# Performance work log

Hardware: AMD Instinct MI355X
Metric: run time of the kernel (lower is better)

## Reference

```python
import jax, jax.numpy as jnp
import numpy as np

EMBED_DIM = 1024
NUM_HEADS = 16
HEAD_DIM = EMBED_DIM // NUM_HEADS
SCALE = HEAD_DIM ** -0.5


def setup_inputs() -> dict:
    key = jax.random.key(0)
    ks = jax.random.split(key, 12)
    B, S, D = 2, 2048, EMBED_DIM
    w_std = D ** -0.5
    return {
        "query": jax.random.normal(ks[0], (B, S, D), jnp.float32),
        "key": jax.random.normal(ks[1], (B, S, D), jnp.float32),
        "value": jax.random.normal(ks[2], (B, S, D), jnp.float32),
        "mask": jnp.ones((B, S, S), jnp.int32),
        "Wq": jax.random.normal(ks[3], (D, D), jnp.float32) * w_std,
        "bq": jnp.zeros((D,), jnp.float32),
        "Wk": jax.random.normal(ks[4], (D, D), jnp.float32) * w_std,
        "bk": jnp.zeros((D,), jnp.float32),
        "Wv": jax.random.normal(ks[5], (D, D), jnp.float32) * w_std,
        "bv": jnp.zeros((D,), jnp.float32),
        "Wo": jax.random.normal(ks[6], (D, D), jnp.float32) * w_std,
        "bo": jnp.zeros((D,), jnp.float32),
    }


def reference(query, key, value, mask, Wq, bq, Wk, bk, Wv, bv, Wo, bo):
    B, Sq, D = query.shape
    H, Hd = NUM_HEADS, HEAD_DIM
    # projections (torch Linear: x @ W.T + b), then split heads -> [B, H, S, Hd]
    q = (query @ Wq.T + bq).reshape(B, Sq, H, Hd).transpose(0, 2, 1, 3)
    k = (key @ Wk.T + bk).reshape(B, -1, H, Hd).transpose(0, 2, 1, 3)
    v = (value @ Wv.T + bv).reshape(B, -1, H, Hd).transpose(0, 2, 1, 3)
    # scaled dot-product scores [B, H, Sq, Sk]
    scores = jnp.einsum("bhqd,bhkd->bhqk", q, k) * SCALE
    scores = jnp.where(mask[:, None, :, :] == 0, -1e9, scores)
    attn_weights = jax.nn.softmax(scores, axis=-1)
    # dropout rate = 0.0 -> identity in this configuration
    attn_output = jnp.einsum("bhqk,bhkd->bhqd", attn_weights, v)
    attn_output = attn_output.transpose(0, 2, 1, 3).reshape(B, Sq, D)
    output = attn_output @ Wo.T + bo
    return (output, attn_weights)
```

## Files before the change

kernel.cpp:

```cpp
#include <hip/hip_runtime.h>
#include <stdint.h>

#define B_ 2
#define S_ 2048
#define D_ 1024
#define H_ 16
#define HD_ 64
#define NT_ (S_ / 64)
#define SC2_ 0.18033688011112042f

typedef __bf16 bf16_t;
typedef bf16_t bf16x8 __attribute__((ext_vector_type(8)));
typedef float f32x4 __attribute__((ext_vector_type(4)));
typedef unsigned short u16x8 __attribute__((ext_vector_type(8)));
typedef unsigned short u16x4 __attribute__((ext_vector_type(4)));

static __device__ __forceinline__ unsigned short f2b(float f) {
  return __builtin_bit_cast(unsigned short, (bf16_t)f);
}

static __device__ __forceinline__ bf16x8 asb(u16x8 u) {
  return __builtin_bit_cast(bf16x8, u);
}

__global__ void cast3(const float* __restrict__ a, const float* __restrict__ b,
                      const float* __restrict__ c,
                      unsigned short* __restrict__ dst, int n) {
  const float* src = blockIdx.y == 0 ? a : (blockIdx.y == 1 ? b : c);
  unsigned short* d = dst + (size_t)blockIdx.y * n;
  int i = (blockIdx.x * blockDim.x + threadIdx.x) * 8;
  if (i >= n) return;
  float4 f0 = *(const float4*)(src + i);
  float4 f1 = *(const float4*)(src + i + 4);
  u16x8 o;
  o[0] = f2b(f0.x); o[1] = f2b(f0.y); o[2] = f2b(f0.z); o[3] = f2b(f0.w);
  o[4] = f2b(f1.x); o[5] = f2b(f1.y); o[6] = f2b(f1.z); o[7] = f2b(f1.w);
  *(u16x8*)(d + i) = o;
}

__global__ void cast4(const float* __restrict__ a, const float* __restrict__ b,
                      const float* __restrict__ c, const float* __restrict__ e,
                      unsigned short* __restrict__ dst, int n) {
  const float* src = blockIdx.y == 0 ? a
                   : (blockIdx.y == 1 ? b : (blockIdx.y == 2 ? c : e));
  unsigned short* d = dst + (size_t)blockIdx.y * n;
  int i = (blockIdx.x * blockDim.x + threadIdx.x) * 8;
  if (i >= n) return;
  float4 f0 = *(const float4*)(src + i);
  float4 f1 = *(const float4*)(src + i + 4);
  u16x8 o;
  o[0] = f2b(f0.x); o[1] = f2b(f0.y); o[2] = f2b(f0.z); o[3] = f2b(f0.w);
  o[4] = f2b(f1.x); o[5] = f2b(f1.y); o[6] = f2b(f1.z); o[7] = f2b(f1.w);
  *(u16x8*)(d + i) = o;
}

__global__ void pack_mask(const int* __restrict__ mask,
                          uint32_t* __restrict__ mbits) {
  int i = blockIdx.x * blockDim.x + threadIdx.x;
  unsigned long long bits = __ballot(mask[i] != 0);
  if ((threadIdx.x & 63) == 0)
    *(unsigned long long*)&mbits[i >> 5] = bits;
}

template<int OUTMODE>
__global__ __launch_bounds__(256)
void gemm_bt(const unsigned short* __restrict__ Ab,
             const unsigned short* __restrict__ Wb,
             const float* __restrict__ bq_,
             const float* __restrict__ bk_,
             const float* __restrict__ bv_,
             void* __restrict__ outv,
             int M, int N, int K) {
  const int z = blockIdx.z;
  const unsigned short* A = Ab + (size_t)z * M * K;
  const unsigned short* W = Wb + (size_t)z * N * K;
  const float* bias = z == 0 ? bq_ : (z == 1 ? bk_ : bv_);

  __shared__ __align__(16) unsigned short As[128 * 40];
  __shared__ __align__(16) unsigned short Bs[128 * 40];

  const int tid = threadIdx.x;
  const int lane = tid & 63;
  const int wave = tid >> 6;
  const int wm = wave >> 1, wn = wave & 1;
  const int row0 = blockIdx.x * 128;
  const int col0 = blockIdx.y * 128;

  const int srow = tid >> 2;
  const int scol = (tid & 3) * 8;
  const int lr = lane & 15;
  const int lg = lane >> 4;
  const int lk = lg * 8;

  f32x4 acc[4][4] = {};

  u16x8 a0 = *(const u16x8*)&A[(size_t)(row0 + srow) * K + scol];
  u16x8 a1 = *(const u16x8*)&A[(size_t)(row0 + srow + 64) * K + scol];
  u16x8 b0 = *(const u16x8*)&W[(size_t)(col0 + srow) * K + scol];
  u16x8 b1 = *(const u16x8*)&W[(size_t)(col0 + srow + 64) * K + scol];

  for (int k0 = 0; k0 < K; k0 += 32) {
    __syncthreads();
    *(u16x8*)&As[srow * 40 + scol] = a0;
    *(u16x8*)&As[(srow + 64) * 40 + scol] = a1;
    *(u16x8*)&Bs[srow * 40 + scol] = b0;
    *(u16x8*)&Bs[(srow + 64) * 40 + scol] = b1;
    if (k0 + 32 < K) {
      a0 = *(const u16x8*)&A[(size_t)(row0 + srow) * K + k0 + 32 + scol];
      a1 = *(const u16x8*)&A[(size_t)(row0 + srow + 64) * K + k0 + 32 + scol];
      b0 = *(const u16x8*)&W[(size_t)(col0 + srow) * K + k0 + 32 + scol];
      b1 = *(const u16x8*)&W[(size_t)(col0 + srow + 64) * K + k0 + 32 + scol];
    }
    __syncthreads();

    bf16x8 af[4], bfr[4];
#pragma unroll
    for (int i = 0; i < 4; ++i)
      af[i] = asb(*(const u16x8*)&As[(wm * 64 + i * 16 + lr) * 40 + lk]);
#pragma unroll
    for (int j = 0; j < 4; ++j)
      bfr[j] = asb(*(const u16x8*)&Bs[(wn * 64 + j * 16 + lr) * 40 + lk]);
#pragma unroll
    for (int i = 0; i < 4; ++i)
#pragma unroll
      for (int j = 0; j < 4; ++j)
        acc[i][j] = __builtin_amdgcn_mfma_f32_16x16x32_bf16(af[i], bfr[j], acc[i][j], 0, 0, 0);
  }

  const size_t zo = (size_t)z * M * N;
#pragma unroll
  for (int i = 0; i < 4; ++i) {
#pragma unroll
    for (int j = 0; j < 4; ++j) {
      const int row_ = row0 + wm * 64 + i * 16 + lg * 4;
      const int col = col0 + wn * 64 + j * 16 + lr;
      const float bcol = bias[col];
      if (OUTMODE == 1) {
        float* O = (float*)outv;
#pragma unroll
        for (int r = 0; r < 4; ++r)
          __builtin_nontemporal_store(acc[i][j][r] + bcol,
                                      &O[(size_t)(row_ + r) * N + col]);
      } else if (z == 2) {
        unsigned short* O = (unsigned short*)outv + zo;
        int b = row_ >> 11, s = row_ & 2047;
        int h = col >> 6, hd = col & 63;
        u16x4 pk;
#pragma unroll
        for (int r = 0; r < 4; ++r) pk[r] = f2b(acc[i][j][r] + bcol);
        *(u16x4*)&O[(((size_t)b * H_ + h) * HD_ + hd) * S_ + s] = pk;
      } else {
        unsigned short* O = (unsigned short*)outv + zo;
        int h = col >> 6, hd = col & 63;
#pragma unroll
        for (int r = 0; r < 4; ++r) {
          int row = row_ + r;
          int b = row >> 11, s = row & 2047;
          O[(((size_t)b * H_ + h) * S_ + s) * HD_ + hd] = f2b(acc[i][j][r] + bcol);
        }
      }
    }
  }
}

static __device__ __forceinline__ void xcd_map(int& bh, int& qt) {
  int lin = blockIdx.y * 32 + blockIdx.x;
  int xcd = lin & 7, k = lin >> 3;
  bh = (xcd << 2) | (k >> 5);
  qt = k & 31;
}

__global__ __launch_bounds__(512)
void attn_fused(const unsigned short* __restrict__ q_bh,
                const unsigned short* __restrict__ k_bh,
                const unsigned short* __restrict__ vt_g,
                const uint32_t* __restrict__ mbits,
                float* __restrict__ w_out,
                unsigned short* __restrict__ attn_out) {
  int bh, qt;
  xcd_map(bh, qt);
  const int b = bh >> 4, h = bh & (H_ - 1);
  const int q0 = qt * 64;

  __shared__ __align__(16) unsigned char smem[36864];
  unsigned short* Ks = (unsigned short*)smem;
  unsigned short* Vs = Ks + 64 * 72;
  unsigned short* Ps = Vs + 64 * 72;
  float* cs = (float*)smem;
  float2* mls = (float2*)Ps;

  const int tid = threadIdx.x, lane = tid & 63, w = tid >> 6;
  const int wq = w >> 1, wk = w & 1;
  const int srow = tid >> 3, scol = (tid & 7) * 8;
  const int lr = lane & 15, lg = lane >> 4, lk = lg * 8;
  const int sq = q0 + wq * 16 + lr;
  unsigned short* Psw = Ps + w * (16 * 72);

  const unsigned short* qb = q_bh + ((size_t)bh * S_ + sq) * HD_;
  bf16x8 qf0 = asb(*(const u16x8*)&qb[lk]);
  bf16x8 qf1 = asb(*(const u16x8*)&qb[32 + lk]);

  const uint32_t* mrow = mbits + ((size_t)b * S_ + sq) * (S_ / 32);
  const unsigned short* kb = k_bh + (size_t)bh * S_ * HD_;
  const unsigned short* vb = vt_g + (size_t)bh * HD_ * S_;

  float m2 = -__builtin_inff(), l = 0.f;
  {
    u16x8 t0 = *(const u16x8*)&kb[srow * 64 + scol];
    for (int kt = 0; kt < NT_; ++kt) {
      __syncthreads();
      *(u16x8*)&Ks[srow * 72 + scol] = t0;
      if (kt + 1 < NT_) {
        const unsigned short* kn = kb + (kt + 1) * 64 * 64;
        t0 = *(const u16x8*)&kn[srow * 64 + scol];
      }
      __syncthreads();

      uint32_t mw = mrow[kt * 2 + wk];
      const bool full = __all(mw == 0xffffffffu);

      f32x4 sa[2] = {};
#pragma unroll
      for (int jj = 0; jj < 2; ++jj) {
        const int j = wk * 2 + jj;
        bf16x8 kf0 = asb(*(const u16x8*)&Ks[(j * 16 + lr) * 72 + lk]);
        bf16x8 kf1 = asb(*(const u16x8*)&Ks[(j * 16 + lr) * 72 + 32 + lk]);
        sa[jj] = __builtin_amdgcn_mfma_f32_16x16x32_bf16(kf0, qf0, sa[jj], 0, 0, 0);
        sa[jj] = __builtin_amdgcn_mfma_f32_16x16x32_bf16(kf1, qf1, sa[jj], 0, 0, 0);
      }

      float sv[2][4];
      if (full) {
#pragma unroll
        for (int jj = 0; jj < 2; ++jj)
#pragma unroll
          for (int r = 0; r < 4; ++r) sv[jj][r] = sa[jj][r] * SC2_;
      } else {
#pragma unroll
        for (int jj = 0; jj < 2; ++jj)
#pragma unroll
          for (int r = 0; r < 4; ++r) {
            int bit = jj * 16 + lg * 4 + r;
            sv[jj][r] = ((mw >> bit) & 1) ? sa[jj][r] * SC2_ : -3.0e9f;
          }
      }
      float tm = sv[0][0];
#pragma unroll
      for (int jj = 0; jj < 2; ++jj)
#pragma unroll
        for (int r = 0; r < 4; ++r) tm = fmaxf(tm, sv[jj][r]);
      tm = fmaxf(tm, __shfl_xor(tm, 16));
      tm = fmaxf(tm, __shfl_xor(tm, 32));
      float mnew = fmaxf(m2, tm);
      float ss = 0.f;
#pragma unroll
      for (int jj = 0; jj < 2; ++jj)
#pragma unroll
        for (int r = 0; r < 4; ++r)
          ss += __builtin_amdgcn_exp2f(sv[jj][r] - mnew);
      ss += __shfl_xor(ss, 16);
      ss += __shfl_xor(ss, 32);
      l = l * __builtin_amdgcn_exp2f(m2 - mnew) + ss;
      m2 = mnew;
    }
  }

  __syncthreads();
  if (lg == 0) mls[wk * 64 + wq * 16 + lr] = make_float2(m2, l);
  __syncthreads();
  float2 h0 = mls[wq * 16 + lr];
  float2 h1 = mls[64 + wq * 16 + lr];
  const float mn = fmaxf(h0.x, h1.x);
  const float lsum = h0.y * __builtin_amdgcn_exp2f(h0.x - mn) +
                     h1.y * __builtin_amdgcn_exp2f(h1.x - mn);
  const float off = -mn - __builtin_amdgcn_logf(lsum);
  float* wrow = w_out + ((size_t)bh * S_ + sq) * S_;

  u16x8 t0 = *(const u16x8*)&kb[srow * 64 + scol];
  u16x8 v0 = *(const u16x8*)&vb[(size_t)srow * S_ + scol];

  f32x4 oacc[4] = {};

  for (int kt = 0; kt < NT_; ++kt) {
    const int k0 = kt * 64;
    __syncthreads();
    *(u16x8*)&Ks[srow * 72 + scol] = t0;
    *(u16x8*)&Vs[srow * 72 + scol] = v0;
    if (kt + 1 < NT_) {
      t0 = *(const u16x8*)&kb[(k0 + 64 + srow) * 64 + scol];
      v0 = *(const u16x8*)&vb[(size_t)srow * S_ + k0 + 64 + scol];
    }
    __syncthreads();

    uint32_t mw = mrow[kt * 2 + wk];
    const bool full = __all(mw == 0xffffffffu);

    f32x4 sa[2] = {};
#pragma unroll
    for (int jj = 0; jj < 2; ++jj) {
      const int j = wk * 2 + jj;
      bf16x8 kf0 = asb(*(const u16x8*)&Ks[(j * 16 + lr) * 72 + lk]);
      bf16x8 kf1 = asb(*(const u16x8*)&Ks[(j * 16 + lr) * 72 + 32 + lk]);
      sa[jj] = __builtin_amdgcn_mfma_f32_16x16x32_bf16(kf0, qf0, sa[jj], 0, 0, 0);
      sa[jj] = __builtin_amdgcn_mfma_f32_16x16x32_bf16(kf1, qf1, sa[jj], 0, 0, 0);
    }

#pragma unroll
    for (int jj = 0; jj < 2; ++jj) {
      f32x4 pv;
      u16x4 pb;
      if (full) {
#pragma unroll
        for (int r = 0; r < 4; ++r) {
          float p = __builtin_amdgcn_exp2f(fmaf(sa[jj][r], SC2_, off));
          pv[r] = p;
          pb[r] = f2b(p);
        }
      } else {
#pragma unroll
        for (int r = 0; r < 4; ++r) {
          int bit = jj * 16 + lg * 4 + r;
          float x = ((mw >> bit) & 1) ? fmaf(sa[jj][r], SC2_, off) : -3.0e9f;
          float p = __builtin_amdgcn_exp2f(x);
          pv[r] = p;
          pb[r] = f2b(p);
        }
      }
      __builtin_nontemporal_store(pv,
          (f32x4*)&wrow[k0 + wk * 32 + jj * 16 + lg * 4]);
      *(u16x4*)&Psw[lr * 72 + wk * 32 + jj * 16 + lg * 4] = pb;
    }

    bf16x8 pa = asb(*(const u16x8*)&Psw[lr * 72 + wk * 32 + lk]);
#pragma unroll
    for (int j2 = 0; j2 < 4; ++j2) {
      bf16x8 vf = asb(*(const u16x8*)&Vs[(j2 * 16 + lr) * 72 + wk * 32 + lk]);
      oacc[j2] = __builtin_amdgcn_mfma_f32_16x16x32_bf16(pa, vf, oacc[j2], 0, 0, 0);
    }
  }

  __syncthreads();
  const int ci = (wq * 64 + lane) * 17;
  if (wk == 1) {
#pragma unroll
    for (int j2 = 0; j2 < 4; ++j2)
#pragma unroll
      for (int r = 0; r < 4; ++r) cs[ci + j2 * 4 + r] = oacc[j2][r];
  }
  __syncthreads();
  if (wk == 0) {
#pragma unroll
    for (int j2 = 0; j2 < 4; ++j2)
#pragma unroll
      for (int r = 0; r < 4; ++r) {
        float v = oacc[j2][r] + cs[ci + j2 * 4 + r];
        attn_out[((size_t)b * S_ + q0 + wq * 16 + lg * 4 + r) * D_ + h * HD_ + j2 * 16 + lr] =
            f2b(v);
      }
  }
}

extern "C" void kernel_launch(void* const* d_in, const int* in_sizes, int n_in,
                              void* d_out, int out_size, void* d_ws, size_t ws_size,
                              hipStream_t stream) {
  const float* query = (const float*)d_in[0];
  const float* key   = (const float*)d_in[1];
  const float* value = (const float*)d_in[2];
  const int*   mask  = (const int*)d_in[3];
  const float* Wq = (const float*)d_in[4];
  const float* bq = (const float*)d_in[5];
  const float* Wk = (const float*)d_in[6];
  const float* bk = (const float*)d_in[7];
  const float* Wv = (const float*)d_in[8];
  const float* bv = (const float*)d_in[9];
  const float* Wo = (const float*)d_in[10];
  const float* bo = (const float*)d_in[11];

  const int NE = B_ * S_ * D_;
  const int NW = D_ * D_;

  char* ws = (char*)d_ws;
  unsigned short* xin  = (unsigned short*)(ws);
  uint32_t*       mbits = (uint32_t*)(ws + 8388608);
  unsigned short* wbuf = (unsigned short*)(ws + 25165824);
  unsigned short* qkv  = (unsigned short*)(ws + 33554432);
  unsigned short* aout = (unsigned short*)(ws + 59244544);

  cast3<<<dim3(NE / 2048, 3), dim3(256), 0, stream>>>(query, key, value, xin, NE);
  cast4<<<dim3(NW / 2048, 4), dim3(256), 0, stream>>>(Wq, Wk, Wv, Wo, wbuf, NW);

  gemm_bt<0><<<dim3(32, 8, 3), dim3(256), 0, stream>>>(
      xin, wbuf, bq, bk, bv, qkv, 4096, 1024, 1024);

  pack_mask<<<dim3(B_ * S_ * S_ / 256), dim3(256), 0, stream>>>(mask, mbits);

  float* w_out = (float*)d_out + NE;
  attn_fused<<<dim3(32, 32), dim3(512), 0, stream>>>(
      qkv, qkv + NE, qkv + 2 * NE, mbits, w_out, aout);

  gemm_bt<1><<<dim3(32, 8, 1), dim3(256), 0, stream>>>(
      aout, wbuf + 3 * NW, bo, bo, bo, d_out, 4096, 1024, 1024);
}
```

Baseline: 295.5 us.

## Enlarge attention blocks to 128 query rows with 1024 threads

The fused attention kernel now handles 128 query rows per block with 16 waves instead of 64 rows with 8 waves, so each loaded K/V tile is shared by twice as many queries. In the second pass, K and V staging is split between the two halves of the block, and the per-wave P scratch is narrowed to only the 32 columns each wave uses, so shared memory stays the same size. The grid is halved and the XCD mapping is adjusted to match. The aggressive launch bounds (1024, 8) may cap registers and cause spills, and there are fewer blocks in flight.

```diff
diff --git a/kernel.cpp b/kernel.cpp
--- a/kernel.cpp
+++ b/kernel.cpp
@@ -164,13 +164,13 @@
 }
 
 static __device__ __forceinline__ void xcd_map(int& bh, int& qt) {
-  int lin = blockIdx.y * 32 + blockIdx.x;
+  int lin = blockIdx.y * 16 + blockIdx.x;
   int xcd = lin & 7, k = lin >> 3;
-  bh = (xcd << 2) | (k >> 5);
-  qt = k & 31;
-}
-
-__global__ __launch_bounds__(512)
+  bh = (xcd << 2) | (k >> 4);
+  qt = k & 15;
+}
+
+__global__ __launch_bounds__(1024, 8)
 void attn_fused(const unsigned short* __restrict__ q_bh,
                 const unsigned short* __restrict__ k_bh,
                 const unsigned short* __restrict__ vt_g,
@@ -180,7 +180,7 @@
   int bh, qt;
   xcd_map(bh, qt);
   const int b = bh >> 4, h = bh & (H_ - 1);
-  const int q0 = qt * 64;
+  const int q0 = qt * 128;
 
   __shared__ __align__(16) unsigned char smem[36864];
   unsigned short* Ks = (unsigned short*)smem;
@@ -191,10 +191,12 @@
 
   const int tid = threadIdx.x, lane = tid & 63, w = tid >> 6;
   const int wq = w >> 1, wk = w & 1;
-  const int srow = tid >> 3, scol = (tid & 7) * 8;
+  const int sthalf = tid >> 9;
+  const int st = tid & 511;
+  const int srow = st >> 3, scol = (st & 7) * 8;
   const int lr = lane & 15, lg = lane >> 4, lk = lg * 8;
   const int sq = q0 + wq * 16 + lr;
-  unsigned short* Psw = Ps + w * (16 * 72);
+  unsigned short* Psw = Ps + w * (16 * 36);
 
   const unsigned short* qb = q_bh + ((size_t)bh * S_ + sq) * HD_;
   bf16x8 qf0 = asb(*(const u16x8*)&qb[lk]);
@@ -206,13 +208,14 @@
 
   float m2 = -__builtin_inff(), l = 0.f;
   {
-    u16x8 t0 = *(const u16x8*)&kb[srow * 64 + scol];
+    u16x8 t0;
+    if (sthalf == 0) t0 = *(const u16x8*)&kb[srow * 64 + scol];
     for (int kt = 0; kt < NT_; ++kt) {
       __syncthreads();
-      *(u16x8*)&Ks[srow * 72 + scol] = t0;
-      if (kt + 1 < NT_) {
-        const unsigned short* kn = kb + (kt + 1) * 64 * 64;
-        t0 = *(const u16x8*)&kn[srow * 64 + scol];
+      if (sthalf == 0) {
+        *(u16x8*)&Ks[srow * 72 + scol] = t0;
+        if (kt + 1 < NT_)
+          t0 = *(const u16x8*)&kb[((kt + 1) * 64 + srow) * 64 + scol];
       }
       __syncthreads();
 
@@ -266,29 +269,30 @@
   }
 
   __syncthreads();
-  if (lg == 0) mls[wk * 64 + wq * 16 + lr] = make_float2(m2, l);
+  if (lg == 0) mls[wk * 128 + wq * 16 + lr] = make_float2(m2, l);
   __syncthreads();
   float2 h0 = mls[wq * 16 + lr];
-  float2 h1 = mls[64 + wq * 16 + lr];
+  float2 h1 = mls[128 + wq * 16 + lr];
   const float mn = fmaxf(h0.x, h1.x);
   const float lsum = h0.y * __builtin_amdgcn_exp2f(h0.x - mn) +
                      h1.y * __builtin_amdgcn_exp2f(h1.x - mn);
   const float off = -mn - __builtin_amdgcn_logf(lsum);
   float* wrow = w_out + ((size_t)bh * S_ + sq) * S_;
 
-  u16x8 t0 = *(const u16x8*)&kb[srow * 64 + scol];
-  u16x8 v0 = *(const u16x8*)&vb[(size_t)srow * S_ + scol];
+  u16x8 s0;
+  if (sthalf == 0) s0 = *(const u16x8*)&kb[srow * 64 + scol];
+  else             s0 = *(const u16x8*)&vb[(size_t)srow * S_ + scol];
 
   f32x4 oacc[4] = {};
 
   for (int kt = 0; kt < NT_; ++kt) {
     const int k0 = kt * 64;
     __syncthreads();
-    *(u16x8*)&Ks[srow * 72 + scol] = t0;
-    *(u16x8*)&Vs[srow * 72 + scol] = v0;
+    if (sthalf == 0) *(u16x8*)&Ks[srow * 72 + scol] = s0;
+    else             *(u16x8*)&Vs[srow * 72 + scol] = s0;
     if (kt + 1 < NT_) {
-      t0 = *(const u16x8*)&kb[(k0 + 64 + srow) * 64 + scol];
-      v0 = *(const u16x8*)&vb[(size_t)srow * S_ + k0 + 64 + scol];
+      if (sthalf == 0) s0 = *(const u16x8*)&kb[(k0 + 64 + srow) * 64 + scol];
+      else             s0 = *(const u16x8*)&vb[(size_t)srow * S_ + k0 + 64 + scol];
     }
     __syncthreads();
 
@@ -328,10 +332,10 @@
       }
       __builtin_nontemporal_store(pv,
           (f32x4*)&wrow[k0 + wk * 32 + jj * 16 + lg * 4]);
-      *(u16x4*)&Psw[lr * 72 + wk * 32 + jj * 16 + lg * 4] = pb;
-    }
-
-    bf16x8 pa = asb(*(const u16x8*)&Psw[lr * 72 + wk * 32 + lk]);
+      *(u16x4*)&Psw[lr * 36 + jj * 16 + lg * 4] = pb;
+    }
+
+    bf16x8 pa = asb(*(const u16x8*)&Psw[lr * 36 + lk]);
 #pragma unroll
     for (int j2 = 0; j2 < 4; ++j2) {
       bf16x8 vf = asb(*(const u16x8*)&Vs[(j2 * 16 + lr) * 72 + wk * 32 + lk]);
@@ -395,7 +399,7 @@
   pack_mask<<<dim3(B_ * S_ * S_ / 256), dim3(256), 0, stream>>>(mask, mbits);
 
   float* w_out = (float*)d_out + NE;
-  attn_fused<<<dim3(32, 32), dim3(512), 0, stream>>>(
+  attn_fused<<<dim3(16, 32), dim3(1024), 0, stream>>>(
       qkv, qkv + NE, qkv + 2 * NE, mbits, w_out, aout);
 
   gemm_bt<1><<<dim3(32, 8, 1), dim3(256), 0, stream>>>(
```

New measurement: 308.2 us. +4.3%, slower.
